# Kernel tuning notes

Hardware: AMD Instinct MI355X
Metric: run time of the kernel (lower is better)

## Reference

```python
import jax, jax.numpy as jnp
import numpy as np

E = 2048        # embed_dim
H = 16          # num_heads
D = 128         # head_dim
K = 4           # num_hyper_nodes (timelines)
N = 4096        # seq_len
B = 1           # batch (module asserts batch==1)
CAP_FACTOR = 1.25
CAP = int(N / K * CAP_FACTOR)   # 1280, static
ROPE_BASE = 10000.0
SCALE = D ** -0.5
NEG_INF = jnp.float32(-1e30)


def setup_inputs() -> dict:
    key = jax.random.key(0)
    ks = jax.random.split(key, 10)
    def xavier(k, shape):
        fan_in, fan_out = shape[0], shape[1]
        lim = np.sqrt(6.0 / (fan_in + fan_out))
        return jax.random.uniform(k, shape, jnp.float32, -lim, lim)
    return {
        'x':   jax.random.normal(ks[0], (B, N, E), jnp.float32),
        # weights stored (in, out); equivalent to torch Linear weight.T
        'Wq':  xavier(ks[1], (E, H * D)),
        'Wk':  xavier(ks[2], (E, H * D)),
        'Wv':  xavier(ks[3], (E, H * D)),
        'Wo':  xavier(ks[4], (H * D, E)),
        'Wr1': xavier(ks[5], (E, E // 2)),
        'br1': jnp.zeros((E // 2,), jnp.float32),
        'Wr2': xavier(ks[6], (E // 2, K)),
        'br2': jnp.zeros((K,), jnp.float32),
    }


def _rope_tables():
    # local positions: arange(CAP) (use_local_rope=True)
    inv_freq = 1.0 / (ROPE_BASE ** (jnp.arange(0, D, 2, dtype=jnp.float32) / D))
    freqs = jnp.arange(CAP, dtype=jnp.float32)[:, None] * inv_freq[None, :]  # (CAP, D/2)
    emb = jnp.concatenate([freqs, freqs], axis=-1)  # (CAP, D)
    return jnp.cos(emb), jnp.sin(emb)


def _rotate_half(t):
    return jnp.concatenate([-t[..., D // 2:], t[..., :D // 2]], axis=-1)


def reference(x, Wq, Wk, Wv, Wo, Wr1, br1, Wr2, br2):
    # --- expert-choice routing ---
    h = jax.nn.gelu(x @ Wr1 + br1, approximate=False)      # (B, N, E/2)
    scores = h @ Wr2 + br2                                  # (B, N, K)
    scores_t = scores[0].T                                  # (K, N)
    topk_scores, topk_idx = jax.lax.top_k(scores_t, CAP)    # (K, CAP)
    sel_w = jax.nn.softmax(topk_scores, axis=-1)            # (K, CAP)
    aux_loss = -jnp.mean(jnp.max(scores, axis=-1))

    # --- projections ---
    q = (x @ Wq).reshape(B, N, H, D).transpose(0, 2, 1, 3)  # (B, H, N, D)
    k = (x @ Wk).reshape(B, N, H, D).transpose(0, 2, 1, 3)
    v = (x @ Wv).reshape(B, N, H, D).transpose(0, 2, 1, 3)

    cos, sin = _rope_tables()                               # (CAP, D)
    causal = jnp.tril(jnp.ones((CAP, CAP), bool))

    def timeline(idx, w):
        # gather this timeline's tokens
        qt = q[:, :, idx]                                   # (B, H, CAP, D)
        kt = k[:, :, idx]
        vt = v[:, :, idx]
        qt = qt * cos + _rotate_half(qt) * sin
        kt = kt * cos + _rotate_half(kt) * sin
        att = jnp.einsum('bhqd,bhkd->bhqk', qt, kt) * SCALE
        att = jnp.where(causal, att, NEG_INF)
        att = jax.nn.softmax(att, axis=-1)
        o = jnp.einsum('bhqk,bhkd->bhqd', att, vt)          # (B, H, CAP, D)
        return o * w[None, None, :, None]                   # weighted combine

    outs = jax.vmap(timeline)(topk_idx, sel_w)              # (K, B, H, CAP, D)

    # scatter back: sum contributions over timelines
    idx_flat = topk_idx.reshape(-1)                         # (K*CAP,)
    vals = outs.transpose(1, 2, 0, 3, 4).reshape(B, H, K * CAP, D)
    out = jnp.zeros((B, H, N, D), x.dtype).at[:, :, idx_flat, :].add(vals)

    out = out.transpose(0, 2, 1, 3).reshape(B, N, H * D) @ Wo  # (B, N, E)
    return out, aux_loss
```

## Files before the change

kernel.cpp:

```cpp
#include <hip/hip_runtime.h>
#include <cstdint>
#include <cstddef>

#define N_TOK 4096
#define E_DIM 2048
#define NH    16
#define DH    128
#define KEXP  4
#define CAPN  1280
#define NTILE 20
#define QKV_STRIDE 6144
#define SCALE_QK 0.08838834764831845f
#define LOG2E    1.4426950408889634f
#define NEG_BIG -1e30f

typedef __attribute__((ext_vector_type(4))) float f32x4;
typedef __attribute__((ext_vector_type(8))) short s16x8;

__device__ __forceinline__ float bf2f(unsigned short u){
  union{unsigned int i; float fl;} c; c.i = ((unsigned int)u)<<16; return c.fl;
}
__device__ __forceinline__ unsigned short f2bf(float x){
  union{float fl; unsigned int i;} c; c.fl=x;
  return (unsigned short)((c.i + 0x7FFFu + ((c.i>>16)&1u))>>16);
}
__device__ __forceinline__ f32x4 mfma_bf16(s16x8 a, s16x8 b, f32x4 c){
  asm("v_mfma_f32_16x16x32_bf16 %0, %1, %2, %0" : "+v"(c) : "v"(a), "v"(b));
  return c;
}
__device__ __forceinline__ void gl_lds16(const unsigned short* g, unsigned short* l){
  __builtin_amdgcn_global_load_lds(
      (const __attribute__((address_space(1))) unsigned int*)g,
      (__attribute__((address_space(3))) unsigned int*)l, 16, 0, 0);
}

__global__ __launch_bounds__(256) void conv_x_kernel(const float* __restrict__ x,
    unsigned short* __restrict__ hi, unsigned short* __restrict__ lo, int n4){
  int idx = blockIdx.x*256 + threadIdx.x;
  if (idx >= n4) return;
  float4 v = ((const float4*)x)[idx];
  float ar[4] = {v.x, v.y, v.z, v.w};
  union{ unsigned short u[4]; uint2 q; } H, L;
  #pragma unroll
  for(int i=0;i<4;i++){
    unsigned short h = f2bf(ar[i]);
    H.u[i] = h;
    L.u[i] = f2bf(ar[i] - bf2f(h));
  }
  ((uint2*)hi)[idx] = H.q;
  ((uint2*)lo)[idx] = L.q;
}

__global__ __launch_bounds__(256) void tconv_kernel(const float* __restrict__ W,
    unsigned short* __restrict__ Thi, unsigned short* __restrict__ Tlo, int R, int C){
  __shared__ float t[32][33];
  int tx = threadIdx.x, ty = threadIdx.y;
  int c0 = blockIdx.x*32, r0 = blockIdx.y*32;
  #pragma unroll
  for(int i=0;i<4;i++){
    int r = r0 + ty + i*8;
    t[ty+i*8][tx] = W[(size_t)r*C + c0 + tx];
  }
  __syncthreads();
  #pragma unroll
  for(int i=0;i<4;i++){
    int c = c0 + ty + i*8;
    float v = t[tx][ty+i*8];
    size_t o = (size_t)c*R + r0 + tx;
    unsigned short h = f2bf(v);
    Thi[o] = h;
    if (Tlo) Tlo[o] = f2bf(v - bf2f(h));
  }
}

__global__ __launch_bounds__(256) void tconv4_kernel(const float* __restrict__ W0,
    const float* __restrict__ W1, const float* __restrict__ W2, const float* __restrict__ W3,
    unsigned short* __restrict__ out){
  __shared__ float t[32][33];
  int z = blockIdx.z;
  const float* W = (z==0)?W0 : (z==1)?W1 : (z==2)?W2 : W3;
  unsigned short* T = out + (size_t)z*E_DIM*E_DIM;
  int tx = threadIdx.x, ty = threadIdx.y;
  int c0 = blockIdx.x*32, r0 = blockIdx.y*32;
  #pragma unroll
  for(int i=0;i<4;i++){
    int r = r0 + ty + i*8;
    t[ty+i*8][tx] = W[(size_t)r*E_DIM + c0 + tx];
  }
  __syncthreads();
  #pragma unroll
  for(int i=0;i<4;i++){
    int c = c0 + ty + i*8;
    T[(size_t)c*E_DIM + r0 + tx] = f2bf(t[tx][ty+i*8]);
  }
}

template<int OUTBF>
__global__ __launch_bounds__(512, 1) void gemm_p(
    const unsigned short* __restrict__ A, const unsigned short* __restrict__ Bt,
    void* __restrict__ Cp, int N, int Kd){
  __shared__ __align__(16) unsigned short lds[2][24576];
  const int tid = threadIdx.x;
  const int w = tid>>6, lane = tid&63, g = lane>>4, r16 = lane&15;
  const int wm = w>>2, wn = w&3;
  const int mb = blockIdx.y, nb = blockIdx.x;
  const unsigned short* Ab = A  + (size_t)mb*128*Kd;
  const unsigned short* Bb = Bt + (size_t)nb*256*Kd;
  const int NT = Kd >> 6;

  f32x4 acc[4][4];
  #pragma unroll
  for(int i=0;i<4;i++)
    #pragma unroll
    for(int j=0;j<4;j++) acc[i][j] = f32x4{0.f,0.f,0.f,0.f};

  auto stageA = [&](int buf, int ks, int t){
    int row = tid>>2, ch = tid&3;
    int sc = ch ^ ((row>>1)&3);
    gl_lds16(Ab + (size_t)row*Kd + t*64 + ks*32 + sc*8, &lds[buf][ks*4096 + tid*8]);
  };
  auto stageB = [&](int buf, int ks, int t){
    #pragma unroll
    for(int i=0;i<2;i++){
      int n = i*512 + tid;
      int row = n>>2, ch = n&3;
      int sc = ch ^ ((row>>1)&3);
      gl_lds16(Bb + (size_t)row*Kd + t*64 + ks*32 + sc*8, &lds[buf][8192 + ks*8192 + n*8]);
    }
  };
  const int xoff = (g ^ ((r16>>1)&3)) << 3;

  stageA(0,0,0); stageB(0,0,0);
  stageA(0,1,0); stageB(0,1,0);
  stageA(1,0,1); stageB(1,0,1);
  asm volatile("s_waitcnt vmcnt(6)" ::: "memory");
  __builtin_amdgcn_s_barrier();

  int cur = 0;
  for(int t=0; t<NT; ++t){
    const int nxt = cur^1;
    s16x8 af[4], bfv[4];
    #pragma unroll
    for(int mf=0;mf<4;mf++)
      af[mf] = *(const s16x8*)&lds[cur][(wm*64 + mf*16 + r16)*32 + xoff];
    #pragma unroll
    for(int nf=0;nf<4;nf++)
      bfv[nf] = *(const s16x8*)&lds[cur][8192 + (wn*64 + nf*16 + r16)*32 + xoff];
    if (t+1 < NT){
      stageA(nxt,1,t+1); stageB(nxt,1,t+1);
      asm volatile("s_waitcnt vmcnt(6)" ::: "memory");
    } else {
      asm volatile("s_waitcnt vmcnt(0)" ::: "memory");
    }
    __builtin_amdgcn_s_barrier();
    __builtin_amdgcn_s_setprio(1);
    #pragma unroll
    for(int mf=0;mf<4;mf++)
      #pragma unroll
      for(int nf=0;nf<4;nf++)
        acc[mf][nf] = mfma_bf16(af[mf], bfv[nf], acc[mf][nf]);
    __builtin_amdgcn_s_setprio(0);
    __builtin_amdgcn_s_barrier();
    #pragma unroll
    for(int mf=0;mf<4;mf++)
      af[mf] = *(const s16x8*)&lds[cur][4096 + (wm*64 + mf*16 + r16)*32 + xoff];
    #pragma unroll
    for(int nf=0;nf<4;nf++)
      bfv[nf] = *(const s16x8*)&lds[cur][16384 + (wn*64 + nf*16 + r16)*32 + xoff];
    if (t+2 < NT){
      stageA(cur,0,t+2); stageB(cur,0,t+2);
      asm volatile("s_waitcnt vmcnt(6)" ::: "memory");
    } else if (t+1 < NT){
      asm volatile("s_waitcnt vmcnt(3)" ::: "memory");
    } else {
      asm volatile("s_waitcnt vmcnt(0)" ::: "memory");
    }
    __builtin_amdgcn_s_barrier();
    __builtin_amdgcn_s_setprio(1);
    #pragma unroll
    for(int mf=0;mf<4;mf++)
      #pragma unroll
      for(int nf=0;nf<4;nf++)
        acc[mf][nf] = mfma_bf16(af[mf], bfv[nf], acc[mf][nf]);
    __builtin_amdgcn_s_setprio(0);
    __builtin_amdgcn_s_barrier();
    cur ^= 1;
  }

  const int rowb = mb*128 + wm*64, colb = nb*256 + wn*64;
  #pragma unroll
  for(int mf=0;mf<4;mf++)
    #pragma unroll
    for(int nf=0;nf<4;nf++)
      #pragma unroll
      for(int r=0;r<4;r++){
        int rr = rowb + mf*16 + 4*g + r;
        int cc = colb + nf*16 + r16;
        size_t o = (size_t)rr*N + cc;
        if (OUTBF) ((unsigned short*)Cp)[o] = f2bf(acc[mf][nf][r]);
        else       ((float*)Cp)[o] = acc[mf][nf][r];
      }
}

__global__ __launch_bounds__(256) void gemm_router_kernel(
    const unsigned short* __restrict__ Ahi, const unsigned short* __restrict__ Alo,
    const unsigned short* __restrict__ Bhi, const unsigned short* __restrict__ Blo,
    const float* __restrict__ br1, float* __restrict__ H){
  __shared__ __align__(16) unsigned short AsH[128*32];
  __shared__ __align__(16) unsigned short AsL[128*32];
  __shared__ __align__(16) unsigned short BsH[128*32];
  __shared__ __align__(16) unsigned short BsL[128*32];
  const int mb = blockIdx.y, nb = blockIdx.x;
  const int tid = threadIdx.x;
  const int lane = tid & 63, w = tid >> 6;
  const int g = lane >> 4, r16 = lane & 15;
  const int wm = w >> 1, wn = w & 1;
  f32x4 acc[4][4];
  #pragma unroll
  for(int i=0;i<4;i++)
    #pragma unroll
    for(int j=0;j<4;j++) acc[i][j] = f32x4{0.f,0.f,0.f,0.f};
  const unsigned short* AbH = Ahi + (size_t)mb*128*E_DIM;
  const unsigned short* AbL = Alo + (size_t)mb*128*E_DIM;
  const unsigned short* BbH = Bhi + (size_t)nb*128*E_DIM;
  const unsigned short* BbL = Blo + (size_t)nb*128*E_DIM;
  const int xr2 = (r16>>1)&3;
  for(int k0=0;k0<E_DIM;k0+=32){
    __syncthreads();
    #pragma unroll
    for(int i=0;i<2;i++){
      int c = i*256 + tid;
      int row = c>>2;
      int sc = ((c&3) ^ ((row>>1)&3))*8;
      size_t go = (size_t)row*E_DIM + k0 + sc;
      gl_lds16(AbH + go, &AsH[c*8]);
      gl_lds16(AbL + go, &AsL[c*8]);
      gl_lds16(BbH + go, &BsH[c*8]);
      gl_lds16(BbL + go, &BsL[c*8]);
    }
    __syncthreads();
    s16x8 ah[4], al[4], bh[4], bl[4];
    #pragma unroll
    for(int f2=0;f2<4;f2++){
      int ra = (wm*64 + f2*16 + r16)*32 + 8*(g ^ xr2);
      int rb = (wn*64 + f2*16 + r16)*32 + 8*(g ^ xr2);
      ah[f2] = *(const s16x8*)&AsH[ra];
      al[f2] = *(const s16x8*)&AsL[ra];
      bh[f2] = *(const s16x8*)&BsH[rb];
      bl[f2] = *(const s16x8*)&BsL[rb];
    }
    #pragma unroll
    for(int fm=0;fm<4;fm++)
      #pragma unroll
      for(int fn=0;fn<4;fn++){
        acc[fm][fn] = mfma_bf16(ah[fm], bh[fn], acc[fm][fn]);
        acc[fm][fn] = mfma_bf16(ah[fm], bl[fn], acc[fm][fn]);
        acc[fm][fn] = mfma_bf16(al[fm], bh[fn], acc[fm][fn]);
      }
  }
  const int rowb = mb*128 + wm*64, colb = nb*128 + wn*64;
  #pragma unroll
  for(int fm=0;fm<4;fm++)
    #pragma unroll
    for(int fn=0;fn<4;fn++)
      #pragma unroll
      for(int r=0;r<4;r++){
        int rr = rowb + fm*16 + 4*g + r;
        int cc = colb + fn*16 + r16;
        float v = acc[fm][fn][r] + br1[cc];
        H[(size_t)rr*1024 + cc] = 0.5f*v*(1.0f + erff(v*0.70710678118654752f));
      }
}

__global__ __launch_bounds__(256) void scores_kernel(const float* __restrict__ h,
    const float* __restrict__ Wr2, const float* __restrict__ br2,
    float* __restrict__ scores, float* __restrict__ tokmax){
  int tid = threadIdx.x;
  int n = blockIdx.x*4 + (tid>>6);
  int lane = tid & 63;
  const float* hr = h + (size_t)n*1024;
  float s0=0,s1=0,s2=0,s3=0;
  #pragma unroll
  for(int i=0;i<16;i++){
    int j = lane + i*64;
    float hv = hr[j];
    float4 wv = *(const float4*)(Wr2 + (size_t)j*4);
    s0 += hv*wv.x; s1 += hv*wv.y; s2 += hv*wv.z; s3 += hv*wv.w;
  }
  #pragma unroll
  for(int m=32;m>=1;m>>=1){
    s0 += __shfl_xor(s0,m); s1 += __shfl_xor(s1,m);
    s2 += __shfl_xor(s2,m); s3 += __shfl_xor(s3,m);
  }
  if (lane==0){
    s0+=br2[0]; s1+=br2[1]; s2+=br2[2]; s3+=br2[3];
    scores[n*4+0]=s0; scores[n*4+1]=s1; scores[n*4+2]=s2; scores[n*4+3]=s3;
    tokmax[n]=fmaxf(fmaxf(s0,s1),fmaxf(s2,s3));
  }
}

__global__ __launch_bounds__(1024) void aux_kernel(const float* __restrict__ tokmax, float* __restrict__ out_aux){
  __shared__ float red[1024];
  int t = threadIdx.x;
  red[t] = tokmax[t] + tokmax[t+1024] + tokmax[t+2048] + tokmax[t+3072];
  __syncthreads();
  for(int k=512;k>=1;k>>=1){ if(t<k) red[t]+=red[t+k]; __syncthreads(); }
  if (t==0) out_aux[0] = -red[0]/4096.0f;
}

__global__ __launch_bounds__(1024) void topk_kernel(const float* __restrict__ scores,
    int* __restrict__ topk_idx, float* __restrict__ sel_w, int* __restrict__ rank_of){
  __shared__ float sv[4096];
  __shared__ int   si[4096];
  __shared__ float red[1024];
  int e = blockIdx.x, t = threadIdx.x;
  for(int i=t;i<4096;i+=1024){ sv[i]=scores[i*4+e]; si[i]=i; }
  __syncthreads();
  for(int k=2;k<=4096;k<<=1){
    for(int j=k>>1;j>0;j>>=1){
      for(int i=t;i<4096;i+=1024){
        int ixj = i^j;
        if (ixj>i){
          float vi=sv[i], vj=sv[ixj];
          int ii=si[i], ij=si[ixj];
          bool jGreater = (vj>vi) || (vj==vi && ij<ii);
          bool asc = (i&k)==0;
          if (asc ? jGreater : !jGreater){
            sv[i]=vj; sv[ixj]=vi; si[i]=ij; si[ixj]=ii;
          }
        }
      }
      __syncthreads();
    }
  }
  for(int i=t;i<4096;i+=1024) rank_of[e*4096+i] = -1;
  __syncthreads();
  for(int r=t;r<CAPN;r+=1024){
    int tok = si[r];
    topk_idx[e*CAPN+r] = tok;
    rank_of[e*4096+tok] = r;
  }
  float mx = sv[0];
  float part = 0.f;
  for(int r=t;r<CAPN;r+=1024) part += expf(sv[r]-mx);
  red[t]=part; __syncthreads();
  for(int k=512;k>=1;k>>=1){ if(t<k) red[t]+=red[t+k]; __syncthreads(); }
  float denom = red[0];
  for(int r=t;r<CAPN;r+=1024) sel_w[e*CAPN+r] = expf(sv[r]-mx)/denom;
}

__global__ __launch_bounds__(256) void rope_kernel(float* __restrict__ cosT, float* __restrict__ sinT){
  int idx = blockIdx.x*256 + threadIdx.x;
  int p = idx>>6, dm = idx&63;
  float inv = powf(10000.0f, -(float)dm/64.0f);
  float ang = (float)p*inv;
  cosT[idx]=cosf(ang);
  sinT[idx]=sinf(ang);
}

__global__ __launch_bounds__(256) void prerope_k_kernel(const unsigned short* __restrict__ kb,
    const int* __restrict__ topk_idx, const float* __restrict__ cosT, const float* __restrict__ sinT,
    unsigned short* __restrict__ Kg){
  int idx = blockIdx.x*256 + threadIdx.x;
  int ch = idx & 15;
  int rest = idx >> 4;
  int rank = rest % CAPN;
  int he = rest / CAPN;
  int e = he >> 4, h = he & 15;
  int tok = topk_idx[e*CAPN + rank];
  int d0 = ch*8;
  const unsigned short* krow = kb + (size_t)tok*QKV_STRIDE + h*DH;
  unsigned short held[8], part[8];
  *(uint4*)held = *(const uint4*)(krow + d0);
  *(uint4*)part = *(const uint4*)(krow + (d0^64));
  const float* cr = cosT + rank*64;
  const float* sr = sinT + rank*64;
  float sgn = (d0<64) ? -1.f : 1.f;
  unsigned short outv[8];
  #pragma unroll
  for(int jj=0;jj<8;jj++){
    int dm = (d0+jj)&63;
    outv[jj] = f2bf(bf2f(held[jj])*cr[dm] + sgn*bf2f(part[jj])*sr[dm]);
  }
  int t = rank >> 6, row = rank & 63;
  size_t tbase = ((size_t)(he)*NTILE + t) * 8192;
  *(uint4*)(Kg + tbase + row*128 + ((ch ^ (row&7))<<3)) = *(uint4*)outv;
}

__global__ __launch_bounds__(256) void prev_kernel(const unsigned short* __restrict__ vb,
    const int* __restrict__ topk_idx, unsigned short* __restrict__ Vg){
  __shared__ __align__(16) unsigned short T2[128][72];
  int bid = blockIdx.x;
  int t = bid % NTILE, h = (bid/NTILE) & 15, e = bid/(NTILE*NH);
  int tid = threadIdx.x, lane = tid & 63, dchb = tid >> 6;
  int tok = topk_idx[e*CAPN + t*64 + lane];
  const unsigned short* vrow = vb + (size_t)tok*QKV_STRIDE + h*DH;
  #pragma unroll
  for(int i=0;i<4;i++){
    int d0 = (dchb + i*4)*8;
    unsigned short vv[8];
    *(uint4*)vv = *(const uint4*)(vrow + d0);
    #pragma unroll
    for(int j=0;j<8;j++) T2[d0+j][lane] = vv[j];
  }
  __syncthreads();
  unsigned short* out = Vg + ((size_t)(e*NH+h)*NTILE + t)*8192;
  #pragma unroll
  for(int i=0;i<4;i++){
    int c = i*256 + tid;
    int d = c>>3, ch = c&7;
    *(uint4*)(out + d*64 + ((ch ^ (d&7))<<3)) = *(const uint4*)&T2[d][ch*8];
  }
}

__global__ __launch_bounds__(256) void attn_kernel(
    const unsigned short* __restrict__ qb,
    const unsigned short* __restrict__ Kg, const unsigned short* __restrict__ Vg,
    const int* __restrict__ topk_idx, const float* __restrict__ sel_w,
    const float* __restrict__ cosT, const float* __restrict__ sinT,
    unsigned short* __restrict__ oexp){
  __shared__ __align__(16) unsigned short KsA[2][8192];
  __shared__ __align__(16) unsigned short Vs[8192];
  __shared__ __align__(16) unsigned short Ps[4][16][72];
  const int id = blockIdx.x;
  const int xcd = id & 7, s_ = id >> 3;
  const int qt = NTILE - 1 - (s_ % NTILE);
  const int grp = (s_ / NTILE)*8 + xcd;
  const int e = grp >> 4, hh = grp & 15;
  const int tid = threadIdx.x, w = tid>>6, lane = tid&63, g = lane>>4, r16 = lane&15;
  const int* idxE = topk_idx + e*CAPN;
  const unsigned short* Kgb = Kg + (size_t)(e*NH+hh)*CAPN*DH;
  const unsigned short* Vgb = Vg + (size_t)(e*NH+hh)*CAPN*DH;

  s16x8 aq[4];
  {
    int qr = qt*64 + w*16 + r16;
    int tok = idxE[qr];
    const unsigned short* qrow = qb + (size_t)tok*QKV_STRIDE + hh*DH;
    const float* cr = cosT + qr*64;
    const float* sr = sinT + qr*64;
    #pragma unroll
    for(int s=0;s<4;s++){
      int d0 = s*32 + 8*g;
      unsigned short held[8], part[8];
      *(uint4*)held = *(const uint4*)(qrow + d0);
      *(uint4*)part = *(const uint4*)(qrow + (d0^64));
      float sgn = (d0<64) ? -1.f : 1.f;
      union{ s16x8 v; unsigned short u[8]; } fr;
      #pragma unroll
      for(int jj=0;jj<8;jj++){
        int dm = (d0+jj)&63;
        float val = bf2f(held[jj])*cr[dm] + sgn*bf2f(part[jj])*sr[dm];
        fr.u[jj] = f2bf(val * (SCALE_QK*LOG2E));
      }
      aq[s] = fr.v;
    }
  }
  float m_r[4], l_r[4];
  f32x4 o[8];
  #pragma unroll
  for(int r=0;r<4;r++){ m_r[r]=-INFINITY; l_r[r]=0.f; }
  #pragma unroll
  for(int f2=0;f2<8;f2++) o[f2]=f32x4{0.f,0.f,0.f,0.f};

  #pragma unroll
  for(int i=0;i<4;i++){ int c=i*256+tid; gl_lds16(Kgb + c*8, &KsA[0][c*8]); }
  #pragma unroll
  for(int i=0;i<4;i++){ int c=i*256+tid; gl_lds16(Vgb + c*8, &Vs[c*8]); }
  asm volatile("s_waitcnt vmcnt(4)" ::: "memory");
  __builtin_amdgcn_s_barrier();

  for(int kt=0; kt<=qt; kt++){
    const int cur = kt & 1;
    if (kt < qt){
      const unsigned short* Ksrc = Kgb + (size_t)(kt+1)*8192;
      #pragma unroll
      for(int i=0;i<4;i++){ int c=i*256+tid; gl_lds16(Ksrc + c*8, &KsA[cur^1][c*8]); }
    }
    f32x4 sfr[4];
    #pragma unroll
    for(int fc=0;fc<4;fc++){
      f32x4 a4 = f32x4{0.f,0.f,0.f,0.f};
      const int row = fc*16 + r16;
      #pragma unroll
      for(int s=0;s<4;s++){
        s16x8 bk = *(const s16x8*)&KsA[cur][row*128 + (((s*4+g) ^ (r16&7))<<3)];
        a4 = mfma_bf16(aq[s], bk, a4);
      }
      sfr[fc] = a4;
    }
    if (kt==qt){
      #pragma unroll
      for(int fc=0;fc<4;fc++)
        #pragma unroll
        for(int r=0;r<4;r++){
          int qrank  = qt*64 + w*16 + 4*g + r;
          int kvrank = kt*64 + fc*16 + r16;
          if (kvrank > qrank) sfr[fc][r] = NEG_BIG;
        }
    }
    float corr[4];
    bool need = false;
    #pragma unroll
    for(int r=0;r<4;r++){
      float mx = fmaxf(fmaxf(sfr[0][r],sfr[1][r]), fmaxf(sfr[2][r],sfr[3][r]));
      #pragma unroll
      for(int mk=1;mk<16;mk<<=1) mx = fmaxf(mx, __shfl_xor(mx,mk));
      float nm = fmaxf(m_r[r], mx);
      need = need || (nm > m_r[r]);
      corr[r] = exp2f(m_r[r]-nm);
      m_r[r] = nm;
    }
    if (__any(need)){
      #pragma unroll
      for(int f2=0;f2<8;f2++)
        #pragma unroll
        for(int r=0;r<4;r++) o[f2][r] *= corr[r];
      #pragma unroll
      for(int r=0;r<4;r++) l_r[r] *= corr[r];
    }
    float rs[4] = {0.f,0.f,0.f,0.f};
    #pragma unroll
    for(int fc=0;fc<4;fc++)
      #pragma unroll
      for(int r=0;r<4;r++){
        float p = exp2f(sfr[fc][r] - m_r[r]);
        rs[r] += p;
        Ps[w][4*g+r][fc*16+r16] = f2bf(p);
      }
    #pragma unroll
    for(int r=0;r<4;r++){
      float ts = rs[r];
      #pragma unroll
      for(int mk=1;mk<16;mk<<=1) ts += __shfl_xor(ts,mk);
      l_r[r] += ts;
    }
    if (kt < qt) asm volatile("s_waitcnt vmcnt(4)" ::: "memory");
    else         asm volatile("s_waitcnt vmcnt(0)" ::: "memory");
    __builtin_amdgcn_s_barrier();
    #pragma unroll
    for(int ks=0;ks<2;ks++){
      s16x8 pa = *(const s16x8*)&Ps[w][r16][ks*32 + 8*g];
      #pragma unroll
      for(int fd=0;fd<8;fd++){
        const int row = fd*16 + r16;
        s16x8 vf = *(const s16x8*)&Vs[row*64 + (((ks*4+g) ^ (r16&7))<<3)];
        o[fd] = mfma_bf16(pa, vf, o[fd]);
      }
    }
    __builtin_amdgcn_s_barrier();
    if (kt < qt){
      const unsigned short* Vsrc = Vgb + (size_t)(kt+1)*8192;
      #pragma unroll
      for(int i=0;i<4;i++){ int c=i*256+tid; gl_lds16(Vsrc + c*8, &Vs[c*8]); }
      asm volatile("s_waitcnt vmcnt(4)" ::: "memory");
      __builtin_amdgcn_s_barrier();
    }
  }
  #pragma unroll
  for(int r=0;r<4;r++){
    int qrank = qt*64 + w*16 + 4*g + r;
    float fac = sel_w[e*CAPN + qrank] / l_r[r];
    #pragma unroll
    for(int fd=0;fd<8;fd++){
      oexp[((size_t)(e*CAPN + qrank))*E_DIM + hh*DH + fd*16 + r16] = f2bf(o[fd][r]*fac);
    }
  }
}

__global__ __launch_bounds__(256) void acc_kernel(const unsigned short* __restrict__ oexp,
    const int* __restrict__ rank_of, unsigned short* __restrict__ accb){
  int n = blockIdx.x, t = threadIdx.x;
  int base = t*8;
  float s[8] = {0,0,0,0,0,0,0,0};
  #pragma unroll
  for(int e=0;e<4;e++){
    int r = rank_of[e*4096+n];
    if (r>=0){
      union{uint4 q; unsigned short u[8];} ld;
      ld.q = *(const uint4*)(oexp + ((size_t)(e*CAPN+r))*E_DIM + base);
      #pragma unroll
      for(int j2=0;j2<8;j2++) s[j2] += bf2f(ld.u[j2]);
    }
  }
  union{uint4 q; unsigned short u[8];} st;
  #pragma unroll
  for(int j2=0;j2<8;j2++) st.u[j2] = f2bf(s[j2]);
  *(uint4*)(accb + (size_t)n*E_DIM + base) = st.q;
}

extern "C" void kernel_launch(void* const* d_in, const int* in_sizes, int n_in,
                              void* d_out, int out_size, void* d_ws, size_t ws_size,
                              hipStream_t stream) {
  const float* x   = (const float*)d_in[0];
  const float* Wq  = (const float*)d_in[1];
  const float* Wk  = (const float*)d_in[2];
  const float* Wv  = (const float*)d_in[3];
  const float* Wo  = (const float*)d_in[4];
  const float* Wr1 = (const float*)d_in[5];
  const float* br1 = (const float*)d_in[6];
  const float* Wr2 = (const float*)d_in[7];
  const float* br2 = (const float*)d_in[8];

  char* ws = (char*)d_ws;
  size_t off = 0;
  auto alloc = [&](size_t bytes)->void*{
    void* p = ws + off;
    off += (bytes + 255) & ~(size_t)255;
    return p;
  };
  unsigned short* xhi   = (unsigned short*)alloc((size_t)N_TOK*E_DIM*2);
  unsigned short* xlo   = (unsigned short*)alloc((size_t)N_TOK*E_DIM*2);
  unsigned short* wr1hi = (unsigned short*)alloc((size_t)E_DIM*1024*2);
  unsigned short* wr1lo = (unsigned short*)alloc((size_t)E_DIM*1024*2);
  unsigned short* wqkvT = (unsigned short*)alloc((size_t)3*E_DIM*E_DIM*2);
  unsigned short* woT   = (unsigned short*)alloc((size_t)E_DIM*E_DIM*2);
  void* hv = alloc((size_t)KEXP*NH*CAPN*DH*2);
  float* hbuf = (float*)hv;
  unsigned short* Vg = (unsigned short*)hv;
  float* scores = (float*)alloc((size_t)N_TOK*4*4);
  float* tokmax = (float*)alloc((size_t)N_TOK*4);
  int*   topkI  = (int*)alloc((size_t)KEXP*CAPN*4);
  float* selw   = (float*)alloc((size_t)KEXP*CAPN*4);
  int*   rankof = (int*)alloc((size_t)KEXP*N_TOK*4);
  float* cosT   = (float*)alloc((size_t)CAPN*64*4);
  float* sinT   = (float*)alloc((size_t)CAPN*64*4);
  unsigned short* qkvbuf = (unsigned short*)alloc((size_t)N_TOK*QKV_STRIDE*2);
  unsigned short* oexp = (unsigned short*)alloc((size_t)KEXP*CAPN*E_DIM*2);
  unsigned short* accb = (unsigned short*)alloc((size_t)N_TOK*E_DIM*2);
  if (off > ws_size) return;

  unsigned short* Kg = xlo;

  conv_x_kernel<<<(N_TOK*E_DIM/4+255)/256, 256, 0, stream>>>(x, xhi, xlo, N_TOK*E_DIM/4);
  tconv_kernel<<<dim3(1024/32, E_DIM/32), dim3(32,8), 0, stream>>>(Wr1, wr1hi, wr1lo, E_DIM, 1024);
  tconv4_kernel<<<dim3(E_DIM/32, E_DIM/32, 4), dim3(32,8), 0, stream>>>(Wq, Wk, Wv, Wo, wqkvT);

  gemm_router_kernel<<<dim3(8, 32), 256, 0, stream>>>(xhi, xlo, wr1hi, wr1lo, br1, hbuf);
  scores_kernel<<<N_TOK/4, 256, 0, stream>>>(hbuf, Wr2, br2, scores, tokmax);
  aux_kernel<<<1, 1024, 0, stream>>>(tokmax, ((float*)d_out) + (size_t)N_TOK*E_DIM);
  topk_kernel<<<KEXP, 1024, 0, stream>>>(scores, topkI, selw, rankof);
  rope_kernel<<<CAPN*64/256, 256, 0, stream>>>(cosT, sinT);

  gemm_p<1><<<dim3(QKV_STRIDE/256, N_TOK/128), 512, 0, stream>>>(xhi, wqkvT, qkvbuf, QKV_STRIDE, E_DIM);

  prerope_k_kernel<<<KEXP*NH*CAPN*16/256, 256, 0, stream>>>(qkvbuf + E_DIM, topkI, cosT, sinT, Kg);
  prev_kernel<<<KEXP*NH*NTILE, 256, 0, stream>>>(qkvbuf + 2*E_DIM, topkI, Vg);

  attn_kernel<<<KEXP*NH*NTILE, 256, 0, stream>>>(qkvbuf, Kg, Vg, topkI, selw, cosT, sinT, oexp);

  acc_kernel<<<N_TOK, 256, 0, stream>>>(oexp, rankof, accb);

  gemm_p<0><<<dim3(E_DIM/256, N_TOK/128), 512, 0, stream>>>(accb, woT, (float*)d_out, E_DIM, E_DIM);
}
```

Measured before the change: 478.5 us.

## Pipeline router GEMM with double-buffered LDS and replace bitonic top-k with rank counting

Rewrites the router GEMM to use 512 threads with double-buffered LDS staging, vmcnt-based waits and s_setprio around the MFMA block, so global loads overlap compute. It also replaces the single-block-per-expert bitonic sort with a parallel rank-counting kernel that spreads 16 blocks per expert, plus a separate softmax kernel for selection weights. Rank counting is O(N^2) comparisons per expert but runs across many blocks instead of serialized sort stages, and it adds one extra launch.

```diff
diff --git a/kernel.cpp b/kernel.cpp
--- a/kernel.cpp
+++ b/kernel.cpp
@@ -202,72 +202,94 @@
       }
 }
 
-__global__ __launch_bounds__(256) void gemm_router_kernel(
+__global__ __launch_bounds__(512, 1) void gemm_router_p(
     const unsigned short* __restrict__ Ahi, const unsigned short* __restrict__ Alo,
     const unsigned short* __restrict__ Bhi, const unsigned short* __restrict__ Blo,
     const float* __restrict__ br1, float* __restrict__ H){
-  __shared__ __align__(16) unsigned short AsH[128*32];
-  __shared__ __align__(16) unsigned short AsL[128*32];
-  __shared__ __align__(16) unsigned short BsH[128*32];
-  __shared__ __align__(16) unsigned short BsL[128*32];
+  __shared__ __align__(16) unsigned short lds[2][32768];
+  const int tid = threadIdx.x;
+  const int w = tid>>6, lane = tid&63, g = lane>>4, r16 = lane&15;
+  const int wm = w>>2, wn = w&3;
   const int mb = blockIdx.y, nb = blockIdx.x;
-  const int tid = threadIdx.x;
-  const int lane = tid & 63, w = tid >> 6;
-  const int g = lane >> 4, r16 = lane & 15;
-  const int wm = w >> 1, wn = w & 1;
-  f32x4 acc[4][4];
-  #pragma unroll
-  for(int i=0;i<4;i++)
-    #pragma unroll
-    for(int j=0;j<4;j++) acc[i][j] = f32x4{0.f,0.f,0.f,0.f};
   const unsigned short* AbH = Ahi + (size_t)mb*128*E_DIM;
   const unsigned short* AbL = Alo + (size_t)mb*128*E_DIM;
   const unsigned short* BbH = Bhi + (size_t)nb*128*E_DIM;
   const unsigned short* BbL = Blo + (size_t)nb*128*E_DIM;
-  const int xr2 = (r16>>1)&3;
-  for(int k0=0;k0<E_DIM;k0+=32){
-    __syncthreads();
-    #pragma unroll
-    for(int i=0;i<2;i++){
-      int c = i*256 + tid;
-      int row = c>>2;
-      int sc = ((c&3) ^ ((row>>1)&3))*8;
-      size_t go = (size_t)row*E_DIM + k0 + sc;
-      gl_lds16(AbH + go, &AsH[c*8]);
-      gl_lds16(AbL + go, &AsL[c*8]);
-      gl_lds16(BbH + go, &BsH[c*8]);
-      gl_lds16(BbL + go, &BsL[c*8]);
-    }
-    __syncthreads();
-    s16x8 ah[4], al[4], bh[4], bl[4];
-    #pragma unroll
-    for(int f2=0;f2<4;f2++){
-      int ra = (wm*64 + f2*16 + r16)*32 + 8*(g ^ xr2);
-      int rb = (wn*64 + f2*16 + r16)*32 + 8*(g ^ xr2);
-      ah[f2] = *(const s16x8*)&AsH[ra];
-      al[f2] = *(const s16x8*)&AsL[ra];
-      bh[f2] = *(const s16x8*)&BsH[rb];
-      bl[f2] = *(const s16x8*)&BsL[rb];
-    }
-    #pragma unroll
-    for(int fm=0;fm<4;fm++)
-      #pragma unroll
-      for(int fn=0;fn<4;fn++){
-        acc[fm][fn] = mfma_bf16(ah[fm], bh[fn], acc[fm][fn]);
-        acc[fm][fn] = mfma_bf16(ah[fm], bl[fn], acc[fm][fn]);
-        acc[fm][fn] = mfma_bf16(al[fm], bh[fn], acc[fm][fn]);
-      }
-  }
-  const int rowb = mb*128 + wm*64, colb = nb*128 + wn*64;
-  #pragma unroll
-  for(int fm=0;fm<4;fm++)
-    #pragma unroll
-    for(int fn=0;fn<4;fn++)
+  const int NT = E_DIM >> 6;
+
+  f32x4 acc[4][2];
+  #pragma unroll
+  for(int i=0;i<4;i++){ acc[i][0]=f32x4{0.f,0.f,0.f,0.f}; acc[i][1]=f32x4{0.f,0.f,0.f,0.f}; }
+
+  auto stage = [&](int buf, int ks, int t){
+    int row = tid>>2, ch = tid&3;
+    int sc = ch ^ ((row>>1)&3);
+    size_t go = (size_t)row*E_DIM + t*64 + ks*32 + sc*8;
+    unsigned short* base = &lds[buf][ks*16384];
+    gl_lds16(AbH + go, base +         tid*8);
+    gl_lds16(AbL + go, base +  4096 + tid*8);
+    gl_lds16(BbH + go, base +  8192 + tid*8);
+    gl_lds16(BbL + go, base + 12288 + tid*8);
+  };
+  const int xoff = (g ^ ((r16>>1)&3)) << 3;
+
+  stage(0,0,0); stage(0,1,0); stage(1,0,1);
+  asm volatile("s_waitcnt vmcnt(8)" ::: "memory");
+  __builtin_amdgcn_s_barrier();
+
+  int cur = 0;
+  for(int t=0; t<NT; ++t){
+    const int nxt = cur^1;
+    #pragma unroll
+    for(int ph=0; ph<2; ph++){
+      const unsigned short* base = &lds[cur][ph*16384];
+      s16x8 ah[4], al[4], bh[2], bl[2];
+      #pragma unroll
+      for(int mf=0;mf<4;mf++){
+        int ro = (wm*64 + mf*16 + r16)*32 + xoff;
+        ah[mf] = *(const s16x8*)&base[ro];
+        al[mf] = *(const s16x8*)&base[4096 + ro];
+      }
+      #pragma unroll
+      for(int nf=0;nf<2;nf++){
+        int ro = (wn*32 + nf*16 + r16)*32 + xoff;
+        bh[nf] = *(const s16x8*)&base[8192 + ro];
+        bl[nf] = *(const s16x8*)&base[12288 + ro];
+      }
+      if (ph==0){
+        if (t+1 < NT){ stage(nxt,1,t+1); asm volatile("s_waitcnt vmcnt(8)" ::: "memory"); }
+        else         {                   asm volatile("s_waitcnt vmcnt(0)" ::: "memory"); }
+      } else {
+        if (t+2 < NT){ stage(cur,0,t+2); asm volatile("s_waitcnt vmcnt(8)" ::: "memory"); }
+        else if (t+1 < NT){              asm volatile("s_waitcnt vmcnt(4)" ::: "memory"); }
+        else              {              asm volatile("s_waitcnt vmcnt(0)" ::: "memory"); }
+      }
+      __builtin_amdgcn_s_barrier();
+      __builtin_amdgcn_s_setprio(1);
+      #pragma unroll
+      for(int mf=0;mf<4;mf++)
+        #pragma unroll
+        for(int nf=0;nf<2;nf++){
+          acc[mf][nf] = mfma_bf16(ah[mf], bh[nf], acc[mf][nf]);
+          acc[mf][nf] = mfma_bf16(ah[mf], bl[nf], acc[mf][nf]);
+          acc[mf][nf] = mfma_bf16(al[mf], bh[nf], acc[mf][nf]);
+        }
+      __builtin_amdgcn_s_setprio(0);
+      __builtin_amdgcn_s_barrier();
+    }
+    cur ^= 1;
+  }
+
+  const int rowb = mb*128 + wm*64, colb = nb*128 + wn*32;
+  #pragma unroll
+  for(int mf=0;mf<4;mf++)
+    #pragma unroll
+    for(int nf=0;nf<2;nf++)
       #pragma unroll
       for(int r=0;r<4;r++){
-        int rr = rowb + fm*16 + 4*g + r;
-        int cc = colb + fn*16 + r16;
-        float v = acc[fm][fn][r] + br1[cc];
+        int rr = rowb + mf*16 + 4*g + r;
+        int cc = colb + nf*16 + r16;
+        float v = acc[mf][nf][r] + br1[cc];
         H[(size_t)rr*1024 + cc] = 0.5f*v*(1.0f + erff(v*0.70710678118654752f));
       }
 }
@@ -308,45 +330,43 @@
   if (t==0) out_aux[0] = -red[0]/4096.0f;
 }
 
-__global__ __launch_bounds__(1024) void topk_kernel(const float* __restrict__ scores,
-    int* __restrict__ topk_idx, float* __restrict__ sel_w, int* __restrict__ rank_of){
-  __shared__ float sv[4096];
-  __shared__ int   si[4096];
+__global__ __launch_bounds__(256) void rank_kernel(const float* __restrict__ scores,
+    int* __restrict__ topk_idx, float* __restrict__ topv, int* __restrict__ rank_of){
+  __shared__ unsigned long long keys[4096];
+  const int e = blockIdx.y, blk = blockIdx.x, tid = threadIdx.x;
+  for(int i=tid;i<4096;i+=256){
+    unsigned u = __float_as_uint(scores[i*4+e]);
+    unsigned m = (u & 0x80000000u) ? ~u : (u | 0x80000000u);
+    keys[i] = (((unsigned long long)m)<<32) | (unsigned)(4095-i);
+  }
+  __syncthreads();
+  const int i = blk*256 + tid;
+  const unsigned long long mykey = keys[i];
+  int cnt = 0;
+  #pragma unroll 8
+  for(int j=0;j<4096;j++) cnt += (keys[j] > mykey) ? 1 : 0;
+  if (cnt < CAPN){
+    topk_idx[e*CAPN + cnt] = i;
+    topv[e*CAPN + cnt]     = scores[i*4+e];
+    rank_of[e*4096 + i]    = cnt;
+  } else {
+    rank_of[e*4096 + i]    = -1;
+  }
+}
+
+__global__ __launch_bounds__(1024) void selw_kernel(const float* __restrict__ topv,
+    float* __restrict__ sel_w){
   __shared__ float red[1024];
-  int e = blockIdx.x, t = threadIdx.x;
-  for(int i=t;i<4096;i+=1024){ sv[i]=scores[i*4+e]; si[i]=i; }
+  const int e = blockIdx.x, t = threadIdx.x;
+  const float mx = topv[e*CAPN];
+  float p0 = expf(topv[e*CAPN + t] - mx);
+  float p1 = (t + 1024 < CAPN) ? expf(topv[e*CAPN + t + 1024] - mx) : 0.f;
+  red[t] = p0 + p1;
   __syncthreads();
-  for(int k=2;k<=4096;k<<=1){
-    for(int j=k>>1;j>0;j>>=1){
-      for(int i=t;i<4096;i+=1024){
-        int ixj = i^j;
-        if (ixj>i){
-          float vi=sv[i], vj=sv[ixj];
-          int ii=si[i], ij=si[ixj];
-          bool jGreater = (vj>vi) || (vj==vi && ij<ii);
-          bool asc = (i&k)==0;
-          if (asc ? jGreater : !jGreater){
-            sv[i]=vj; sv[ixj]=vi; si[i]=ij; si[ixj]=ii;
-          }
-        }
-      }
-      __syncthreads();
-    }
-  }
-  for(int i=t;i<4096;i+=1024) rank_of[e*4096+i] = -1;
-  __syncthreads();
-  for(int r=t;r<CAPN;r+=1024){
-    int tok = si[r];
-    topk_idx[e*CAPN+r] = tok;
-    rank_of[e*4096+tok] = r;
-  }
-  float mx = sv[0];
-  float part = 0.f;
-  for(int r=t;r<CAPN;r+=1024) part += expf(sv[r]-mx);
-  red[t]=part; __syncthreads();
   for(int k=512;k>=1;k>>=1){ if(t<k) red[t]+=red[t+k]; __syncthreads(); }
-  float denom = red[0];
-  for(int r=t;r<CAPN;r+=1024) sel_w[e*CAPN+r] = expf(sv[r]-mx)/denom;
+  const float denom = red[0];
+  sel_w[e*CAPN + t] = p0/denom;
+  if (t + 1024 < CAPN) sel_w[e*CAPN + t + 1024] = p1/denom;
 }
 
 __global__ __launch_bounds__(256) void rope_kernel(float* __restrict__ cosT, float* __restrict__ sinT){
@@ -621,6 +641,7 @@
   float* scores = (float*)alloc((size_t)N_TOK*4*4);
   float* tokmax = (float*)alloc((size_t)N_TOK*4);
   int*   topkI  = (int*)alloc((size_t)KEXP*CAPN*4);
+  float* topv   = (float*)alloc((size_t)KEXP*CAPN*4);
   float* selw   = (float*)alloc((size_t)KEXP*CAPN*4);
   int*   rankof = (int*)alloc((size_t)KEXP*N_TOK*4);
   float* cosT   = (float*)alloc((size_t)CAPN*64*4);
@@ -636,10 +657,11 @@
   tconv_kernel<<<dim3(1024/32, E_DIM/32), dim3(32,8), 0, stream>>>(Wr1, wr1hi, wr1lo, E_DIM, 1024);
   tconv4_kernel<<<dim3(E_DIM/32, E_DIM/32, 4), dim3(32,8), 0, stream>>>(Wq, Wk, Wv, Wo, wqkvT);
 
-  gemm_router_kernel<<<dim3(8, 32), 256, 0, stream>>>(xhi, xlo, wr1hi, wr1lo, br1, hbuf);
+  gemm_router_p<<<dim3(8, 32), 512, 0, stream>>>(xhi, xlo, wr1hi, wr1lo, br1, hbuf);
   scores_kernel<<<N_TOK/4, 256, 0, stream>>>(hbuf, Wr2, br2, scores, tokmax);
   aux_kernel<<<1, 1024, 0, stream>>>(tokmax, ((float*)d_out) + (size_t)N_TOK*E_DIM);
-  topk_kernel<<<KEXP, 1024, 0, stream>>>(scores, topkI, selw, rankof);
+  rank_kernel<<<dim3(16, KEXP), 256, 0, stream>>>(scores, topkI, topv, rankof);
+  selw_kernel<<<KEXP, 1024, 0, stream>>>(topv, selw);
   rope_kernel<<<CAPN*64/256, 256, 0, stream>>>(cosT, sinT);
 
   gemm_p<1><<<dim3(QKV_STRIDE/256, N_TOK/128), 512, 0, stream>>>(xhi, wqkvT, qkvbuf, QKV_STRIDE, E_DIM);
```

Result: faster. 448.3 us (-6.3%).
